# Performance work log

Hardware: AMD Instinct MI355X
Metric: run time of the kernel (lower is better)

Reference implementation:

```python
import jax, jax.numpy as jnp
import numpy as np

NINPUTS = 16
WIDTH = 128
KSIZE = 21
SPP = 8
BS, CI, H, W = 2, 3, 192, 192
EPS = 1e-08


def _conv(x, w, b, padding):
    y = jax.lax.conv_general_dilated(
        x, w, window_strides=(1, 1), padding=padding,
        dimension_numbers=("NCHW", "OIHW", "NCHW"))
    return y + b[None, :, None, None]


def apply_kernels(kernel, radiance, ksize):
    """Per-pixel predicted-kernel conv: fused gather-multiply-reduce over taps.
    kernel: (bs, ksize^2, kh, kw), radiance: (bs, ci, h, w).
    Replicates torch apply_kernels (normalization='sum') without materializing
    the (bs, ci, kh, kw, ksize^2) unfold tile tensor."""
    bs, k2, kh, kw = kernel.shape
    _, ci, h, w = radiance.shape
    needed = kh + ksize - 1
    if needed > h:
        crop = (needed - h) // 2
        if crop > 0:
            kernel = kernel[:, :, crop:-crop, crop:-crop]
        kh, kw = kernel.shape[2], kernel.shape[3]
    else:
        crop = (h - needed) // 2
        if crop > 0:
            radiance = radiance[:, :, crop:-crop, crop:-crop]
    taps = jnp.arange(k2, dtype=jnp.int32)
    dy = taps // ksize
    dx = taps % ksize

    def body(acc, idx):
        patch = jax.lax.dynamic_slice(radiance, (0, 0, dy[idx], dx[idx]),
                                      (bs, ci, kh, kw))
        kv = jax.lax.dynamic_slice_in_dim(kernel, idx, 1, axis=1)  # (bs,1,kh,kw)
        return acc + kv * patch, None

    acc0 = jnp.zeros((bs, ci, kh, kw), radiance.dtype)
    weighted_sum, _ = jax.lax.scan(body, acc0, taps)
    kernel_sum = jnp.sum(kernel, axis=1, keepdims=True)  # (bs,1,kh,kw)
    return weighted_sum, kernel_sum


def setup_inputs() -> dict:
    key = jax.random.key(0)
    ks = jax.random.split(key, 10)
    s = 0.05
    inp = {
        "features": jax.random.normal(ks[0], (BS, SPP, NINPUTS, H, W), jnp.float32),
        "radiance": jax.random.uniform(ks[1], (BS, SPP, CI, H, W), jnp.float32),
        # recurrent conv processor (simplified main_processor): SAME 3x3 conv
        "w_rnn": jax.random.normal(ks[2], (WIDTH, NINPUTS + WIDTH, 3, 3), jnp.float32) * s,
        "b_rnn": jnp.zeros((WIDTH,), jnp.float32),
        "w_k1": jax.random.normal(ks[3], (WIDTH, WIDTH + NINPUTS, 3, 3), jnp.float32) * s,
        "b_k1": jnp.zeros((WIDTH,), jnp.float32),
        "w_k2": jax.random.normal(ks[4], (WIDTH, WIDTH, 3, 3), jnp.float32) * s,
        "b_k2": jnp.zeros((WIDTH,), jnp.float32),
        "w_k3": jax.random.normal(ks[5], (KSIZE * KSIZE, WIDTH, 3, 3), jnp.float32) * s,
        "b_k3": jnp.zeros((KSIZE * KSIZE,), jnp.float32),
    }
    return inp


def reference(features, radiance, w_rnn, b_rnn, w_k1, b_k1, w_k2, b_k2, w_k3, b_k3):
    bs, spp, ci, h, w = radiance.shape
    lrelu = lambda x: jax.nn.leaky_relu(x, 0.01)
    state = jnp.zeros((bs, WIDTH, h, w), features.dtype)
    unnorm = sumw = max_k = None
    for step in range(spp):
        f = features[:, step]  # (bs, ninputs, h, w)
        rnn = lrelu(_conv(jnp.concatenate([f, state], axis=1), w_rnn, b_rnn, "SAME"))
        state = rnn
        nf = jnp.concatenate([rnn, f], axis=1)  # (bs, width+ninputs, h, w)
        k = lrelu(_conv(nf, w_k1, b_k1, "VALID"))
        k = lrelu(_conv(k, w_k2, b_k2, "VALID"))
        k = _conv(k, w_k3, b_k3, "VALID")  # (bs, ksize^2, h-6, w-6), linear out
        # online-softmax (flash-attention-style) running max/exp rescale
        new_max = jnp.max(k.reshape(bs, -1), axis=1).reshape(bs, 1, 1, 1)
        if step == 0:
            max_k = new_max
        else:
            old_max = max_k
            max_k = jnp.maximum(old_max, new_max)
        kern = jnp.exp(k - max_k)
        ws, ksum = apply_kernels(kern, radiance[:, step], KSIZE)
        if step == 0:
            unnorm, sumw = ws, ksum
        else:
            scale = jnp.exp(old_max - max_k)
            unnorm = unnorm * scale + ws
            sumw = sumw * scale + ksum
    return unnorm / (sumw + EPS)
```

## Files before the change

kernel.cpp:

```cpp
#include <hip/hip_runtime.h>
#include <stdint.h>

typedef _Float16 half8 __attribute__((ext_vector_type(8)));
typedef _Float16 half4 __attribute__((ext_vector_type(4)));
typedef __attribute__((ext_vector_type(8))) short short8;
typedef __attribute__((ext_vector_type(4))) float f32x4;
typedef __attribute__((ext_vector_type(16))) float f32x16;

__device__ __forceinline__ unsigned encf(float x){
  uint32_t u = __float_as_uint(x);
  return (u & 0x80000000u) ? ~u : (u | 0x80000000u);
}
__device__ __forceinline__ float decf(unsigned u){
  uint32_t b = (u & 0x80000000u) ? (u & 0x7FFFFFFFu) : ~u;
  return __uint_as_float(b);
}
__device__ __forceinline__ void gload16(const void* g, void* l){
  __builtin_amdgcn_global_load_lds(
      (const __attribute__((address_space(1))) void*)g,
      (__attribute__((address_space(3))) void*)l, 16, 0, 0);
}

__global__ __launch_bounds__(256) void zero_u32(unsigned* __restrict__ p, int n){
  for (int i = blockIdx.x*256 + threadIdx.x; i < n; i += gridDim.x*256) p[i] = 0u;
}

__global__ __launch_bounds__(256) void pack_w(const float* __restrict__ w, _Float16* __restrict__ wp,
                                              int CO, int CI, int COP, int CINP){
  int idx = blockIdx.x*256 + threadIdx.x;
  int total = 9*COP*CINP;
  if (idx >= total) return;
  int ci = idx % CINP;
  int rest = idx / CINP;
  int co = rest % COP;
  int t  = rest / COP;
  float v = 0.f;
  if (co < CO && ci < CI) v = w[((size_t)co*CI + ci)*9 + t];
  int kc = ci >> 4, chl = ci & 15;
  wp[(((size_t)kc*9 + t)*(COP/32) + (co>>5))*512 + (co&31)*16 + chl] = (_Float16)v;
}

__global__ __launch_bounds__(256) void pack_bias(const float* __restrict__ b, float* __restrict__ bp, int n, int npad){
  int i = blockIdx.x*256 + threadIdx.x;
  if (i < npad) bp[i] = (i < n) ? b[i] : 0.f;
}

__global__ __launch_bounds__(256) void pack_feat(const float* __restrict__ f,
                                                 _Float16* __restrict__ rnn_in,
                                                 _Float16* __restrict__ k1_in,
                                                 int copy_state,
                                                 unsigned fbstr, unsigned rbstr, unsigned kbstr){
  int p = blockIdx.x*256 + threadIdx.x;
  if (p >= 36864) return;
  int b = blockIdx.y;
  int y = p / 192, x = p % 192;
  const float* fb = f + (size_t)b*fbstr;
  _Float16* r = rnn_in + (size_t)b*rbstr + ((size_t)(y+1)*194 + (x+1))*160;
  _Float16* k = k1_in  + (size_t)b*kbstr + (size_t)p*160;
  #pragma unroll
  for (int c = 0; c < 16; ++c){
    _Float16 v = (_Float16)fb[c*36864 + p];
    r[c] = v;
    k[128 + c] = v;
  }
  if (copy_state){
    #pragma unroll
    for (int cc = 0; cc < 128; cc += 8)
      *reinterpret_cast<short8*>(r + 16 + cc) = *reinterpret_cast<const short8*>(k + cc);
  }
}

template<int CINP, bool RELU, bool K3>
__global__ __launch_bounds__(128, 2) void conv3(
    const _Float16* __restrict__ X, int Wst, unsigned xbstr,
    const _Float16* __restrict__ Wp, int COP,
    const float* __restrict__ bias,
    _Float16* __restrict__ Y, int Wst_out, int DCP, unsigned ybstr,
    unsigned* __restrict__ slot, int Ho, int Wo,
    int nco_mask, int nco_shift)
{
  constexpr int KC = CINP/16;
  constexpr int ITEMS = 6*34*2;
  __shared__ _Float16 lds[2][ITEMS*8];

  const int tid  = threadIdx.x;
  const int lane = tid & 63;
  const int wid  = tid >> 6;
  const int l31  = lane & 31;
  const int hsel = lane >> 5;
  const int xb   = blockIdx.x * 32;
  const int yb   = blockIdx.y * 4;
  const int co_blk = blockIdx.z & nco_mask;
  const int b      = blockIdx.z >> nco_shift;
  const int co_base = co_blk * 128;

  const _Float16* Xb = X + (size_t)b * xbstr;

  uint32_t goff[4];
  #pragma unroll
  for (int k = 0; k < 4; ++k){
    int item = k*128 + tid;
    if (item < ITEMS){
      int row  = item / 68;
      int rem  = item % 68;
      int col  = rem >> 1;
      int half = rem & 1;
      int pix  = (yb + row)*Wst + xb + col;
      goff[k] = (uint32_t)(((uint32_t)pix*CINP + half*8) * 2);
    } else goff[k] = 0;
  }

  auto stage = [&](int buf, int kc){
    const char* xp = (const char*)Xb + (size_t)kc*32;
    char* lb = (char*)&lds[buf][0];
    #pragma unroll
    for (int k = 0; k < 4; ++k){
      if (k*128 + tid < ITEMS)
        gload16(xp + goff[k], lb + k*2048 + wid*1024);
    }
  };

  uint32_t boffe[4];
  #pragma unroll
  for (int n = 0; n < 4; ++n)
    boffe[n] = (uint32_t)((n*34 + l31)*16 + hsel*8);

  f32x16 acc[4][2] = {};
  const _Float16* wbase = Wp + ((size_t)(co_blk*4 + wid*2))*512 + l31*16 + hsel*8;
  const int NG = COP/32;

  half8 wreg[3][2];
  #pragma unroll
  for (int s3 = 0; s3 < 3; ++s3)
    #pragma unroll
    for (int g = 0; g < 2; ++g)
      wreg[s3][g] = *reinterpret_cast<const half8*>(wbase + ((size_t)s3*NG + g)*512);

  stage(0, 0);
  __syncthreads();
  for (int kc = 0; kc < KC; ++kc){
    if (kc + 1 < KC) stage((kc+1)&1, kc+1);
    const _Float16* lb = &lds[kc&1][0];
    half8 breg[2][4];
    #pragma unroll
    for (int n = 0; n < 4; ++n)
      breg[0][n] = *reinterpret_cast<const half8*>(lb + boffe[n]);
    #pragma unroll
    for (int t = 0; t < 9; ++t){
      const int cur = t & 1, nxt = cur ^ 1;
      if (t < 8){
        const int ky = (t+1)/3, kx = (t+1) - ky*3;
        #pragma unroll
        for (int n = 0; n < 4; ++n)
          breg[nxt][n] = *reinterpret_cast<const half8*>(lb + boffe[n] + (ky*34 + kx)*16);
      }
      #pragma unroll
      for (int n = 0; n < 4; ++n)
        #pragma unroll
        for (int g = 0; g < 2; ++g)
          acc[n][g] = __builtin_amdgcn_mfma_f32_32x32x16_f16(wreg[t%3][g], breg[cur][n], acc[n][g], 0, 0, 0);
      {
        const size_t gt = (size_t)(kc*9 + t + 3);
        #pragma unroll
        for (int g = 0; g < 2; ++g)
          wreg[t%3][g] = *reinterpret_cast<const half8*>(wbase + (gt*NG + g)*512);
      }
    }
    if (kc + 1 < KC) __syncthreads();
  }

  const int x = xb + l31;
  float lmax = -3.0e38f;
  #pragma unroll
  for (int n = 0; n < 4; ++n){
    const int y = yb + n;
    if (y < Ho && x < Wo){
      #pragma unroll
      for (int g = 0; g < 2; ++g){
        #pragma unroll
        for (int q = 0; q < 4; ++q){
          const int cb = co_base + (wid*2 + g)*32 + 4*hsel + 8*q;
          f32x4 bs = *reinterpret_cast<const f32x4*>(bias + cb);
          float v[4];
          #pragma unroll
          for (int j = 0; j < 4; ++j){
            float tv = acc[n][g][q*4 + j] + bs[j];
            if (RELU) tv = tv > 0.f ? tv : 0.01f*tv;
            v[j] = tv;
          }
          if constexpr (!K3){
            half4 pk;
            #pragma unroll
            for (int j = 0; j < 4; ++j) pk[j] = (_Float16)v[j];
            *reinterpret_cast<half4*>(Y + (size_t)b*ybstr + ((size_t)y*Wst_out + x)*DCP + cb) = pk;
          } else {
            _Float16* yp = Y + (size_t)b*ybstr;
            #pragma unroll
            for (int j = 0; j < 4; ++j){
              if (cb + j < 441){
                yp[(size_t)(cb+j)*34596 + (size_t)y*186 + x] = (_Float16)v[j];
                lmax = fmaxf(lmax, v[j]);
              }
            }
          }
        }
      }
    }
  }
  if constexpr (K3){
    #pragma unroll
    for (int o = 32; o > 0; o >>= 1) lmax = fmaxf(lmax, __shfl_xor(lmax, o));
    if (lane == 0) atomicMax(slot + b, encf(lmax));
  }
}

__global__ void update_max(float* __restrict__ st, unsigned* __restrict__ slot, int step){
  int b = threadIdx.x;
  if (b < 2){
    float nm   = decf(slot[b]);
    float oldM = st[2*b];
    float M    = (step == 0) ? nm : fmaxf(oldM, nm);
    st[2*b+1] = (step == 0) ? 0.f : expf(oldM - M);
    st[2*b]   = M;
    slot[b] = 0u;
  }
}

__global__ __launch_bounds__(256) void apply_acc(
    const _Float16* __restrict__ k3out, const float* __restrict__ rad,
    const float* __restrict__ st,
    float* __restrict__ unnorm, float* __restrict__ sumw)
{
  const int tx = threadIdx.x & 63, ty = threadIdx.x >> 6;
  const int x = blockIdx.x*64 + tx;
  const int y = blockIdx.y*4 + ty;
  const int b = blockIdx.z;
  if (x >= 172 || y >= 172) return;
  const float M = st[2*b], scale = st[2*b+1];
  const _Float16* kp = k3out + (size_t)b*15256836 + (size_t)(y+7)*186 + (x+7);
  const float* rb = rad + (size_t)b*884736;
  float a0 = 0.f, a1 = 0.f, a2 = 0.f, aw = 0.f;
  for (int dy = 0; dy < 21; ++dy){
    const float* r0 = rb + (size_t)(y+dy)*192 + x;
    #pragma unroll
    for (int dx = 0; dx < 21; ++dx){
      float w = __expf((float)kp[(size_t)(dy*21+dx)*34596] - M);
      aw += w;
      a0 += w * r0[dx];
      a1 += w * r0[36864 + dx];
      a2 += w * r0[73728 + dx];
    }
  }
  size_t p = (size_t)b*88752 + (size_t)y*172 + x;
  size_t ps = (size_t)b*29584 + (size_t)y*172 + x;
  unnorm[p]        = unnorm[p]*scale        + a0;
  unnorm[p+29584]  = unnorm[p+29584]*scale  + a1;
  unnorm[p+59168]  = unnorm[p+59168]*scale  + a2;
  sumw[ps]         = sumw[ps]*scale         + aw;
}

__global__ __launch_bounds__(256) void finalize_out(const float* __restrict__ unnorm,
                                                    const float* __restrict__ sumw,
                                                    float* __restrict__ out){
  int i = blockIdx.x*256 + threadIdx.x;
  int b = blockIdx.y;
  if (i >= 88752) return;
  int p = i % 29584;
  out[(size_t)b*88752 + i] = unnorm[(size_t)b*88752 + i] / (sumw[(size_t)b*29584 + p] + 1e-8f);
}

extern "C" void kernel_launch(void* const* d_in, const int* in_sizes, int n_in,
                              void* d_out, int out_size, void* d_ws, size_t ws_size,
                              hipStream_t stream) {
  const float* features = (const float*)d_in[0];
  const float* radiance = (const float*)d_in[1];
  const float* w_rnn = (const float*)d_in[2];
  const float* b_rnn = (const float*)d_in[3];
  const float* w_k1  = (const float*)d_in[4];
  const float* b_k1  = (const float*)d_in[5];
  const float* w_k2  = (const float*)d_in[6];
  const float* b_k2  = (const float*)d_in[7];
  const float* w_k3  = (const float*)d_in[8];
  const float* b_k3  = (const float*)d_in[9];
  float* out = (float*)d_out;

  char* ws = (char*)d_ws;
  size_t off = 0;
  auto alloc = [&](size_t bytes)->char*{
    char* p = ws + off;
    off = (off + bytes + 255) & ~(size_t)255;
    return p;
  };
  const size_t WSLACK = 49152;
  _Float16* wp_rnn   = (_Float16*)alloc((size_t)9*128*160*2 + WSLACK);
  _Float16* wp_k1    = (_Float16*)alloc((size_t)9*128*160*2 + WSLACK);
  _Float16* wp_k2    = (_Float16*)alloc((size_t)9*128*128*2 + WSLACK);
  _Float16* wp_k3    = (_Float16*)alloc((size_t)9*512*128*2 + WSLACK);
  float*    bias_k3p = (float*)   alloc((size_t)512*4);
  const unsigned RB = 194u*194u*160u;
  const unsigned KB = (192u*192u+448u)*160u;
  const unsigned K2B = (190u*190u+444u)*128u;
  const unsigned K3B = (194u*188u+256u)*128u;
  const unsigned KOB = 441u*34596u;
  _Float16* rnn_in = (_Float16*)alloc((size_t)2*RB*2);
  _Float16* k1_in  = (_Float16*)alloc((size_t)2*KB*2);
  _Float16* k2_in  = (_Float16*)alloc((size_t)2*K2B*2);
  _Float16* k3_in  = (_Float16*)alloc((size_t)2*K3B*2);
  _Float16* k3_out = (_Float16*)alloc((size_t)2*KOB*2);
  float*    accz   = (float*)   alloc((size_t)236678*4);
  if (off > ws_size) return;

  float*    unnorm = accz;
  float*    sumw   = accz + 177504;
  float*    st     = accz + 236672;
  unsigned* slot   = (unsigned*)(accz + 236676);

  pack_w<<<(9*128*160+255)/256, 256, 0, stream>>>(w_rnn, wp_rnn, 128, 144, 128, 160);
  pack_w<<<(9*128*160+255)/256, 256, 0, stream>>>(w_k1,  wp_k1,  128, 144, 128, 160);
  pack_w<<<(9*128*128+255)/256, 256, 0, stream>>>(w_k2,  wp_k2,  128, 128, 128, 128);
  pack_w<<<(9*512*128+255)/256, 256, 0, stream>>>(w_k3,  wp_k3,  441, 128, 512, 128);
  pack_bias<<<2, 256, 0, stream>>>(b_k3, bias_k3p, 441, 512);

  zero_u32<<<2048, 256, 0, stream>>>((unsigned*)rnn_in, (int)(2*RB/2));
  zero_u32<<<925,  256, 0, stream>>>((unsigned*)accz, 236678);

  for (int s = 0; s < 8; ++s){
    const float* f   = features + (size_t)s*16*36864;
    const float* rad = radiance + (size_t)s*3*36864;
    pack_feat<<<dim3(144,2), 256, 0, stream>>>(f, rnn_in, k1_in, s > 0 ? 1 : 0,
                                               8u*16u*36864u, RB, KB);
    conv3<160,true ,false><<<dim3(6,48,2), 128, 0, stream>>>(
        rnn_in, 194, RB, wp_rnn, 128, b_rnn, k1_in, 192, 160, KB,
        nullptr, 192, 192, 0, 0);
    conv3<160,true ,false><<<dim3(6,48,2), 128, 0, stream>>>(
        k1_in, 192, KB, wp_k1, 128, b_k1, k2_in, 190, 128, K2B,
        nullptr, 190, 190, 0, 0);
    conv3<128,true ,false><<<dim3(6,47,2), 128, 0, stream>>>(
        k2_in, 190, K2B, wp_k2, 128, b_k2, k3_in, 188, 128, K3B,
        nullptr, 188, 188, 0, 0);
    conv3<128,false,true ><<<dim3(6,47,8), 128, 0, stream>>>(
        k3_in, 188, K3B, wp_k3, 512, bias_k3p, k3_out, 0, 0, KOB,
        slot, 186, 186, 3, 2);
    update_max<<<1, 64, 0, stream>>>(st, slot, s);
    apply_acc<<<dim3(3,43,2), 256, 0, stream>>>(k3_out, rad, st, unnorm, sumw);
  }
  finalize_out<<<dim3(347,2), 256, 0, stream>>>(unnorm, sumw, out);
}
```

Baseline: 2.552 ms.

## Stage full input-channel tile into LDS once and drop per-chunk double buffering

The conv3 kernel now loads the whole 6x34 pixel tile across all input channels into shared memory in one pass, instead of double-buffering 16-channel chunks with a barrier after each chunk. The MFMA loop is flattened over every chunk and tap, so there are no intra-loop syncs and B-fragment prefetch crosses chunk boundaries. This removes per-chunk barriers and staging overhead, but raises LDS use (about 52KB for 160 channels), which may cut occupancy below two blocks per CU. Workspace buffer sizes and weight slack are adjusted to match the larger reads.

After: 3.163 ms. 24.0% more time.

```diff
diff --git a/kernel.cpp b/kernel.cpp
--- a/kernel.cpp
+++ b/kernel.cpp
@@ -79,9 +79,11 @@
     unsigned* __restrict__ slot, int Ho, int Wo,
     int nco_mask, int nco_shift)
 {
-  constexpr int KC = CINP/16;
-  constexpr int ITEMS = 6*34*2;
-  __shared__ _Float16 lds[2][ITEMS*8];
+  constexpr int KC   = CINP/16;
+  constexpr int CH   = CINP/8;
+  constexpr int ITEMS = 204*CH;
+  constexpr int NRND  = (ITEMS + 127)/128;
+  __shared__ _Float16 lds[ITEMS*8];
 
   const int tid  = threadIdx.x;
   const int lane = tid & 63;
@@ -95,39 +97,22 @@
   const int co_base = co_blk * 128;
 
   const _Float16* Xb = X + (size_t)b * xbstr;
-
-  uint32_t goff[4];
-  #pragma unroll
-  for (int k = 0; k < 4; ++k){
+  const int NG = COP/32;
+  const _Float16* wbase = Wp + ((size_t)(co_blk*4 + wid*2))*512 + l31*16 + hsel*8;
+
+  #pragma unroll
+  for (int k = 0; k < NRND; ++k){
     int item = k*128 + tid;
-    if (item < ITEMS){
-      int row  = item / 68;
-      int rem  = item % 68;
-      int col  = rem >> 1;
-      int half = rem & 1;
-      int pix  = (yb + row)*Wst + xb + col;
-      goff[k] = (uint32_t)(((uint32_t)pix*CINP + half*8) * 2);
-    } else goff[k] = 0;
-  }
-
-  auto stage = [&](int buf, int kc){
-    const char* xp = (const char*)Xb + (size_t)kc*32;
-    char* lb = (char*)&lds[buf][0];
-    #pragma unroll
-    for (int k = 0; k < 4; ++k){
-      if (k*128 + tid < ITEMS)
-        gload16(xp + goff[k], lb + k*2048 + wid*1024);
-    }
-  };
-
-  uint32_t boffe[4];
-  #pragma unroll
-  for (int n = 0; n < 4; ++n)
-    boffe[n] = (uint32_t)((n*34 + l31)*16 + hsel*8);
-
-  f32x16 acc[4][2] = {};
-  const _Float16* wbase = Wp + ((size_t)(co_blk*4 + wid*2))*512 + l31*16 + hsel*8;
-  const int NG = COP/32;
+    if ((ITEMS % 128 == 0) || (item < ITEMS)){
+      int C   = item / 204;
+      int P   = item - C*204;
+      int row = P / 34;
+      int col = P - row*34;
+      int pix = (yb + row)*Wst + xb + col;
+      gload16((const char*)Xb + ((size_t)pix*CINP + C*8)*2,
+              (char*)lds + k*2048 + wid*1024);
+    }
+  }
 
   half8 wreg[3][2];
   #pragma unroll
@@ -136,37 +121,39 @@
     for (int g = 0; g < 2; ++g)
       wreg[s3][g] = *reinterpret_cast<const half8*>(wbase + ((size_t)s3*NG + g)*512);
 
-  stage(0, 0);
   __syncthreads();
-  for (int kc = 0; kc < KC; ++kc){
-    if (kc + 1 < KC) stage((kc+1)&1, kc+1);
-    const _Float16* lb = &lds[kc&1][0];
-    half8 breg[2][4];
-    #pragma unroll
-    for (int n = 0; n < 4; ++n)
-      breg[0][n] = *reinterpret_cast<const half8*>(lb + boffe[n]);
-    #pragma unroll
-    for (int t = 0; t < 9; ++t){
-      const int cur = t & 1, nxt = cur ^ 1;
-      if (t < 8){
-        const int ky = (t+1)/3, kx = (t+1) - ky*3;
-        #pragma unroll
-        for (int n = 0; n < 4; ++n)
-          breg[nxt][n] = *reinterpret_cast<const half8*>(lb + boffe[n] + (ky*34 + kx)*16);
-      }
+
+  const uint32_t blane = (uint32_t)((hsel*204 + l31)*16);
+  const char* lbase = (const char*)lds + blane;
+
+  f32x16 acc[4][2] = {};
+  half8 breg[2][4];
+  #pragma unroll
+  for (int n = 0; n < 4; ++n)
+    breg[0][n] = *reinterpret_cast<const half8*>(lbase + (n*34)*16);
+
+  #pragma unroll
+  for (int ft = 0; ft < KC*9; ++ft){
+    const int cur = ft & 1, nxt = cur ^ 1;
+    if (ft + 1 < KC*9){
+      const int kc1 = (ft+1)/9, t1 = (ft+1)%9;
+      const int ky1 = t1/3, kx1 = t1 - ky1*3;
+      const uint32_t off1 = (uint32_t)((kc1*2*204 + kx1)*16);
       #pragma unroll
       for (int n = 0; n < 4; ++n)
-        #pragma unroll
-        for (int g = 0; g < 2; ++g)
-          acc[n][g] = __builtin_amdgcn_mfma_f32_32x32x16_f16(wreg[t%3][g], breg[cur][n], acc[n][g], 0, 0, 0);
-      {
-        const size_t gt = (size_t)(kc*9 + t + 3);
-        #pragma unroll
-        for (int g = 0; g < 2; ++g)
-          wreg[t%3][g] = *reinterpret_cast<const half8*>(wbase + (gt*NG + g)*512);
-      }
-    }
-    if (kc + 1 < KC) __syncthreads();
+        breg[nxt][n] = *reinterpret_cast<const half8*>(lbase + off1 + ((n + ky1)*34)*16);
+    }
+    #pragma unroll
+    for (int n = 0; n < 4; ++n)
+      #pragma unroll
+      for (int g = 0; g < 2; ++g)
+        acc[n][g] = __builtin_amdgcn_mfma_f32_32x32x16_f16(wreg[ft%3][g], breg[cur][n], acc[n][g], 0, 0, 0);
+    {
+      const size_t gt = (size_t)(ft + 3);
+      #pragma unroll
+      for (int g = 0; g < 2; ++g)
+        wreg[ft%3][g] = *reinterpret_cast<const half8*>(wbase + (gt*NG + g)*512);
+    }
   }
 
   const int x = xb + l31;
@@ -291,16 +278,16 @@
     off = (off + bytes + 255) & ~(size_t)255;
     return p;
   };
-  const size_t WSLACK = 49152;
+  const size_t WSLACK = 98304;
   _Float16* wp_rnn   = (_Float16*)alloc((size_t)9*128*160*2 + WSLACK);
   _Float16* wp_k1    = (_Float16*)alloc((size_t)9*128*160*2 + WSLACK);
   _Float16* wp_k2    = (_Float16*)alloc((size_t)9*128*128*2 + WSLACK);
   _Float16* wp_k3    = (_Float16*)alloc((size_t)9*512*128*2 + WSLACK);
   float*    bias_k3p = (float*)   alloc((size_t)512*4);
-  const unsigned RB = 194u*194u*160u;
-  const unsigned KB = (192u*192u+448u)*160u;
-  const unsigned K2B = (190u*190u+444u)*128u;
-  const unsigned K3B = (194u*188u+256u)*128u;
+  const unsigned RB  = 194u*194u*160u;
+  const unsigned KB  = (194u*192u+64u)*160u;
+  const unsigned K2B = (194u*190u+64u)*128u;
+  const unsigned K3B = (194u*188u+64u)*128u;
   const unsigned KOB = 441u*34596u;
   _Float16* rnn_in = (_Float16*)alloc((size_t)2*RB*2);
   _Float16* k1_in  = (_Float16*)alloc((size_t)2*KB*2);
```

## Crop final conv to the applied kernel region and trim channel padding

Applied to the files above, without the earlier changes.

The last kernel-regressor conv now computes only the central 172x172 outputs that the per-pixel kernel application actually reads, instead of the full 186x186 map. Output channels are padded to 448 rather than 512, which cuts wasted MFMA work on the 441-channel layer. The conv tiling for this layer is also changed: each block covers 8 rows with 64 output channels, and each wave takes 4 rows. The softmax max is now taken over the cropped region only. That is mathematically harmless because the max cancels in normalisation, but it slightly changes the numerics.

Measured after the change: 2.357 ms. 1.08x faster.

```diff
diff --git a/kernel.cpp b/kernel.cpp
--- a/kernel.cpp
+++ b/kernel.cpp
@@ -77,10 +77,12 @@
     const float* __restrict__ bias,
     _Float16* __restrict__ Y, int Wst_out, int DCP, unsigned ybstr,
     unsigned* __restrict__ slot, int Ho, int Wo,
-    int nco_mask, int nco_shift)
+    int nco)
 {
-  constexpr int KC = CINP/16;
-  constexpr int ITEMS = 6*34*2;
+  constexpr int KC    = CINP/16;
+  constexpr int SROWS = K3 ? 10 : 6;
+  constexpr int ITEMS = SROWS*34*2;
+  constexpr int NRND  = (ITEMS + 127)/128;
   __shared__ _Float16 lds[2][ITEMS*8];
 
   const int tid  = threadIdx.x;
@@ -89,16 +91,19 @@
   const int l31  = lane & 31;
   const int hsel = lane >> 5;
   const int xb   = blockIdx.x * 32;
-  const int yb   = blockIdx.y * 4;
-  const int co_blk = blockIdx.z & nco_mask;
-  const int b      = blockIdx.z >> nco_shift;
-  const int co_base = co_blk * 128;
+  const int yb   = blockIdx.y * (K3 ? 8 : 4);
+  const int co_blk = blockIdx.z % nco;
+  const int b      = blockIdx.z / nco;
 
   const _Float16* Xb = X + (size_t)b * xbstr;
-
-  uint32_t goff[4];
-  #pragma unroll
-  for (int k = 0; k < 4; ++k){
+  const int NG = COP/32;
+  const size_t wtap = (size_t)NG*512;
+  const _Float16* wbase = Wp
+      + ((size_t)(K3 ? (co_blk*2) : (co_blk*4 + wid*2)))*512 + l31*16 + hsel*8;
+
+  uint32_t goff[NRND];
+  #pragma unroll
+  for (int k = 0; k < NRND; ++k){
     int item = k*128 + tid;
     if (item < ITEMS){
       int row  = item / 68;
@@ -114,7 +119,7 @@
     const char* xp = (const char*)Xb + (size_t)kc*32;
     char* lb = (char*)&lds[buf][0];
     #pragma unroll
-    for (int k = 0; k < 4; ++k){
+    for (int k = 0; k < NRND; ++k){
       if (k*128 + tid < ITEMS)
         gload16(xp + goff[k], lb + k*2048 + wid*1024);
     }
@@ -122,24 +127,24 @@
 
   uint32_t boffe[4];
   #pragma unroll
-  for (int n = 0; n < 4; ++n)
-    boffe[n] = (uint32_t)((n*34 + l31)*16 + hsel*8);
+  for (int n = 0; n < 4; ++n){
+    const int row = K3 ? (wid*4 + n) : n;
+    boffe[n] = (uint32_t)((row*34 + l31)*16 + hsel*8);
+  }
 
   f32x16 acc[4][2] = {};
-  const _Float16* wbase = Wp + ((size_t)(co_blk*4 + wid*2))*512 + l31*16 + hsel*8;
-  const int NG = COP/32;
-
   half8 wreg[3][2];
   #pragma unroll
   for (int s3 = 0; s3 < 3; ++s3)
     #pragma unroll
     for (int g = 0; g < 2; ++g)
-      wreg[s3][g] = *reinterpret_cast<const half8*>(wbase + ((size_t)s3*NG + g)*512);
+      wreg[s3][g] = *reinterpret_cast<const half8*>(wbase + (size_t)s3*wtap + g*512);
 
   stage(0, 0);
   __syncthreads();
   for (int kc = 0; kc < KC; ++kc){
     if (kc + 1 < KC) stage((kc+1)&1, kc+1);
+    const _Float16* wt = wbase + (size_t)(kc*9)*wtap;
     const _Float16* lb = &lds[kc&1][0];
     half8 breg[2][4];
     #pragma unroll
@@ -149,22 +154,20 @@
     for (int t = 0; t < 9; ++t){
       const int cur = t & 1, nxt = cur ^ 1;
       if (t < 8){
-        const int ky = (t+1)/3, kx = (t+1) - ky*3;
+        const int ky1 = (t+1)/3, kx1 = (t+1) - ky1*3;
         #pragma unroll
         for (int n = 0; n < 4; ++n)
-          breg[nxt][n] = *reinterpret_cast<const half8*>(lb + boffe[n] + (ky*34 + kx)*16);
+          breg[nxt][n] = *reinterpret_cast<const half8*>(lb + boffe[n] + (ky1*34 + kx1)*16);
       }
       #pragma unroll
       for (int n = 0; n < 4; ++n)
         #pragma unroll
         for (int g = 0; g < 2; ++g)
-          acc[n][g] = __builtin_amdgcn_mfma_f32_32x32x16_f16(wreg[t%3][g], breg[cur][n], acc[n][g], 0, 0, 0);
-      {
-        const size_t gt = (size_t)(kc*9 + t + 3);
-        #pragma unroll
-        for (int g = 0; g < 2; ++g)
-          wreg[t%3][g] = *reinterpret_cast<const half8*>(wbase + (gt*NG + g)*512);
-      }
+          acc[n][g] = __builtin_amdgcn_mfma_f32_32x32x16_f16(
+              wreg[t % 3][g], breg[cur][n], acc[n][g], 0, 0, 0);
+      #pragma unroll
+      for (int g = 0; g < 2; ++g)
+        wreg[t % 3][g] = *reinterpret_cast<const half8*>(wt + (size_t)(t+3)*wtap + g*512);
     }
     if (kc + 1 < KC) __syncthreads();
   }
@@ -173,13 +176,14 @@
   float lmax = -3.0e38f;
   #pragma unroll
   for (int n = 0; n < 4; ++n){
-    const int y = yb + n;
+    const int y = yb + (K3 ? (wid*4 + n) : n);
     if (y < Ho && x < Wo){
       #pragma unroll
       for (int g = 0; g < 2; ++g){
         #pragma unroll
         for (int q = 0; q < 4; ++q){
-          const int cb = co_base + (wid*2 + g)*32 + 4*hsel + 8*q;
+          const int cb = (K3 ? (co_blk*64 + g*32) : (co_blk*128 + (wid*2 + g)*32))
+                         + 4*hsel + 8*q;
           f32x4 bs = *reinterpret_cast<const f32x4*>(bias + cb);
           float v[4];
           #pragma unroll
@@ -198,7 +202,7 @@
             #pragma unroll
             for (int j = 0; j < 4; ++j){
               if (cb + j < 441){
-                yp[(size_t)(cb+j)*34596 + (size_t)y*186 + x] = (_Float16)v[j];
+                yp[(size_t)(cb+j)*29584 + (size_t)y*172 + x] = (_Float16)v[j];
                 lmax = fmaxf(lmax, v[j]);
               }
             }
@@ -237,14 +241,14 @@
   const int b = blockIdx.z;
   if (x >= 172 || y >= 172) return;
   const float M = st[2*b], scale = st[2*b+1];
-  const _Float16* kp = k3out + (size_t)b*15256836 + (size_t)(y+7)*186 + (x+7);
+  const _Float16* kp = k3out + (size_t)b*13046544 + (size_t)y*172 + x;
   const float* rb = rad + (size_t)b*884736;
   float a0 = 0.f, a1 = 0.f, a2 = 0.f, aw = 0.f;
   for (int dy = 0; dy < 21; ++dy){
     const float* r0 = rb + (size_t)(y+dy)*192 + x;
     #pragma unroll
     for (int dx = 0; dx < 21; ++dx){
-      float w = __expf((float)kp[(size_t)(dy*21+dx)*34596] - M);
+      float w = __expf((float)kp[(size_t)(dy*21+dx)*29584] - M);
       aw += w;
       a0 += w * r0[dx];
       a1 += w * r0[36864 + dx];
@@ -291,17 +295,17 @@
     off = (off + bytes + 255) & ~(size_t)255;
     return p;
   };
-  const size_t WSLACK = 49152;
+  const size_t WSLACK = 98304;
   _Float16* wp_rnn   = (_Float16*)alloc((size_t)9*128*160*2 + WSLACK);
   _Float16* wp_k1    = (_Float16*)alloc((size_t)9*128*160*2 + WSLACK);
   _Float16* wp_k2    = (_Float16*)alloc((size_t)9*128*128*2 + WSLACK);
-  _Float16* wp_k3    = (_Float16*)alloc((size_t)9*512*128*2 + WSLACK);
-  float*    bias_k3p = (float*)   alloc((size_t)512*4);
-  const unsigned RB = 194u*194u*160u;
-  const unsigned KB = (192u*192u+448u)*160u;
-  const unsigned K2B = (190u*190u+444u)*128u;
-  const unsigned K3B = (194u*188u+256u)*128u;
-  const unsigned KOB = 441u*34596u;
+  _Float16* wp_k3    = (_Float16*)alloc((size_t)9*448*128*2 + WSLACK);
+  float*    bias_k3p = (float*)   alloc((size_t)448*4);
+  const unsigned RB  = 194u*194u*160u;
+  const unsigned KB  = (194u*192u+64u)*160u;
+  const unsigned K2B = (194u*190u+64u)*128u;
+  const unsigned K3B = (194u*188u+64u)*128u;
+  const unsigned KOB = 441u*29584u;
   _Float16* rnn_in = (_Float16*)alloc((size_t)2*RB*2);
   _Float16* k1_in  = (_Float16*)alloc((size_t)2*KB*2);
   _Float16* k2_in  = (_Float16*)alloc((size_t)2*K2B*2);
@@ -318,8 +322,8 @@
   pack_w<<<(9*128*160+255)/256, 256, 0, stream>>>(w_rnn, wp_rnn, 128, 144, 128, 160);
   pack_w<<<(9*128*160+255)/256, 256, 0, stream>>>(w_k1,  wp_k1,  128, 144, 128, 160);
   pack_w<<<(9*128*128+255)/256, 256, 0, stream>>>(w_k2,  wp_k2,  128, 128, 128, 128);
-  pack_w<<<(9*512*128+255)/256, 256, 0, stream>>>(w_k3,  wp_k3,  441, 128, 512, 128);
-  pack_bias<<<2, 256, 0, stream>>>(b_k3, bias_k3p, 441, 512);
+  pack_w<<<(9*448*128+255)/256, 256, 0, stream>>>(w_k3,  wp_k3,  441, 128, 448, 128);
+  pack_bias<<<2, 256, 0, stream>>>(b_k3, bias_k3p, 441, 448);
 
   zero_u32<<<2048, 256, 0, stream>>>((unsigned*)rnn_in, (int)(2*RB/2));
   zero_u32<<<925,  256, 0, stream>>>((unsigned*)accz, 236678);
@@ -331,16 +335,16 @@
                                                8u*16u*36864u, RB, KB);
     conv3<160,true ,false><<<dim3(6,48,2), 128, 0, stream>>>(
         rnn_in, 194, RB, wp_rnn, 128, b_rnn, k1_in, 192, 160, KB,
-        nullptr, 192, 192, 0, 0);
+        nullptr, 192, 192, 1);
     conv3<160,true ,false><<<dim3(6,48,2), 128, 0, stream>>>(
         k1_in, 192, KB, wp_k1, 128, b_k1, k2_in, 190, 128, K2B,
-        nullptr, 190, 190, 0, 0);
+        nullptr, 190, 190, 1);
     conv3<128,true ,false><<<dim3(6,47,2), 128, 0, stream>>>(
         k2_in, 190, K2B, wp_k2, 128, b_k2, k3_in, 188, 128, K3B,
-        nullptr, 188, 188, 0, 0);
-    conv3<128,false,true ><<<dim3(6,47,8), 128, 0, stream>>>(
-        k3_in, 188, K3B, wp_k3, 512, bias_k3p, k3_out, 0, 0, KOB,
-        slot, 186, 186, 3, 2);
+        nullptr, 188, 188, 1);
+    conv3<128,false,true ><<<dim3(6,22,14), 128, 0, stream>>>(
+        k3_in + (size_t)(7*188 + 7)*128, 188, K3B, wp_k3, 448, bias_k3p,
+        k3_out, 0, 0, KOB, slot, 172, 172, 7);
     update_max<<<1, 64, 0, stream>>>(st, slot, s);
     apply_acc<<<dim3(3,43,2), 256, 0, stream>>>(k3_out, rad, st, unnorm, sumw);
   }
```
